# Optimization experiments

Measured on AMD Instinct MI355X. Metric: run time of the kernel, lower is better.

The kernel has to match this reference:

```python
import jax, jax.numpy as jnp
import numpy as np

BATCH = 524288
NUM_DRAFT = 128


def setup_inputs() -> dict:
    key = jax.random.key(0)
    k1, k2 = jax.random.split(key)
    seq_lens = jax.random.randint(k1, (BATCH,), 0, 8192, dtype=jnp.int32)
    evict_mask = jax.random.randint(k2, (BATCH, NUM_DRAFT), 0, 2, dtype=jnp.int32).astype(jnp.bool_)
    return {"seq_lens": seq_lens, "evict_mask": evict_mask, "page_size": 16}


def reference(seq_lens, evict_mask, page_size):
    # seq_lens: [B] int32, evict_mask: [B, D] bool, page_size: python int
    num_draft = evict_mask.shape[1]
    t = jnp.arange(num_draft, dtype=jnp.int32)          # [D]
    num_trues = jnp.sum(evict_mask.astype(jnp.int32), axis=1)   # [B]
    num_false = num_draft - num_trues                    # [B]
    # round (seq_len + num_false) up to page boundary, offset by seq_len
    start = (seq_lens + num_false - 1) // page_size * page_size - seq_lens  # [B]
    start_clamped = jnp.maximum(start, 0)                # [B]
    end = jnp.minimum(start + page_size, num_draft)      # [B] (uses unclamped start)
    range_mask = (t[None, :] >= start_clamped[:, None]) & (t[None, :] < end[:, None])  # [B, D]
    # kernel stores False where range_mask is True
    return jnp.where(range_mask, False, evict_mask)
```

## Files before the change

### kernel.cpp

```cpp
#include <hip/hip_runtime.h>


typedef int vint4 __attribute__((ext_vector_type(4)));

__global__ __launch_bounds__(256) void evict_range_kernel(
    const int* __restrict__ seq_lens,
    const int* __restrict__ evict_mask,
    const int* __restrict__ page_size_p,
    int* __restrict__ out,
    int batch)
{
    const int page = *page_size_p;
    const int lane32 = threadIdx.x & 31;
    const unsigned half_shift = threadIdx.x & 32;
    const int tid = blockIdx.x * blockDim.x + threadIdx.x;
    const int group = tid >> 5;
    const int ngroups = (gridDim.x * blockDim.x) >> 5;

    for (int row = group; row < batch; row += ngroups) {
        const vint4* mrow = reinterpret_cast<const vint4*>(evict_mask) + (size_t)row * 32;
        vint4 v = __builtin_nontemporal_load(&mrow[lane32]);

        unsigned long long b0 = __ballot(v.x != 0);
        unsigned long long b1 = __ballot(v.y != 0);
        unsigned long long b2 = __ballot(v.z != 0);
        unsigned long long b3 = __ballot(v.w != 0);
        int cnt = __popc((unsigned)(b0 >> half_shift))
                + __popc((unsigned)(b1 >> half_shift))
                + __popc((unsigned)(b2 >> half_shift))
                + __popc((unsigned)(b3 >> half_shift));

        int sl = seq_lens[row];
        int num_false = 128 - cnt;
        int s = sl + num_false - 1;
        int q = s / page;
        if (s < 0 && (s % page) != 0) q--;
        int start = q * page - sl;
        int sc  = start > 0 ? start : 0;
        int end = start + page;
        if (end > 128) end = 128;

        int t0 = lane32 * 4;
        vint4 o;
        o.x = (t0 + 0 >= sc && t0 + 0 < end) ? 0 : ((v.x != 0) ? 1 : 0);
        o.y = (t0 + 1 >= sc && t0 + 1 < end) ? 0 : ((v.y != 0) ? 1 : 0);
        o.z = (t0 + 2 >= sc && t0 + 2 < end) ? 0 : ((v.z != 0) ? 1 : 0);
        o.w = (t0 + 3 >= sc && t0 + 3 < end) ? 0 : ((v.w != 0) ? 1 : 0);
        __builtin_nontemporal_store(o, reinterpret_cast<vint4*>(out) + (size_t)row * 32 + lane32);
    }
}

extern "C" void kernel_launch(void* const* d_in, const int* in_sizes, int n_in,
                              void* d_out, int out_size, void* d_ws, size_t ws_size,
                              hipStream_t stream) {
    const int* seq_lens   = (const int*)d_in[0];
    const int* evict_mask = (const int*)d_in[1];
    const int* page_size  = (const int*)d_in[2];
    int* out = (int*)d_out;
    const int batch = in_sizes[0];

    const int blocks = 8192;
    evict_range_kernel<<<blocks, 256, 0, stream>>>(seq_lens, evict_mask, page_size, out, batch);
}
```

Measured before the change: 94.64 us.

## Process two rows per loop iteration, shift-divide for power-of-two pages, fewer blocks

The grid-stride loop now issues loads for two rows before processing either, which puts more memory requests in flight per wavefront. When the page size is a power of two, division is replaced by an arithmetic shift, which also floors correctly for negative values. The grid shrinks from 8192 to 2048 blocks, so each group of 32 threads handles more rows. Fewer resident waves could reduce latency hiding, but the doubled loads in flight are meant to make up for it.

```diff
diff --git a/kernel.cpp b/kernel.cpp
--- a/kernel.cpp
+++ b/kernel.cpp
@@ -2,6 +2,41 @@
 
 
 typedef int vint4 __attribute__((ext_vector_type(4)));
+
+__device__ __forceinline__ void process_row(
+    vint4 v, int sl, int page, int lgp, int lane32, unsigned half_shift,
+    int* __restrict__ out, size_t row)
+{
+    unsigned long long b0 = __ballot(v.x != 0);
+    unsigned long long b1 = __ballot(v.y != 0);
+    unsigned long long b2 = __ballot(v.z != 0);
+    unsigned long long b3 = __ballot(v.w != 0);
+    int cnt = __popc((unsigned)(b0 >> half_shift))
+            + __popc((unsigned)(b1 >> half_shift))
+            + __popc((unsigned)(b2 >> half_shift))
+            + __popc((unsigned)(b3 >> half_shift));
+
+    int s = sl + (128 - cnt) - 1;
+    int q;
+    if (lgp >= 0) {
+        q = s >> lgp;
+    } else {
+        q = s / page;
+        if (s < 0 && (s % page) != 0) q--;
+    }
+    int start = q * page - sl;
+    int sc  = start > 0 ? start : 0;
+    int end = start + page;
+    if (end > 128) end = 128;
+
+    int t0 = lane32 * 4;
+    vint4 o;
+    o.x = (t0 + 0 >= sc && t0 + 0 < end) ? 0 : ((v.x != 0) ? 1 : 0);
+    o.y = (t0 + 1 >= sc && t0 + 1 < end) ? 0 : ((v.y != 0) ? 1 : 0);
+    o.z = (t0 + 2 >= sc && t0 + 2 < end) ? 0 : ((v.z != 0) ? 1 : 0);
+    o.w = (t0 + 3 >= sc && t0 + 3 < end) ? 0 : ((v.w != 0) ? 1 : 0);
+    __builtin_nontemporal_store(o, reinterpret_cast<vint4*>(out) + row * 32 + lane32);
+}
 
 __global__ __launch_bounds__(256) void evict_range_kernel(
     const int* __restrict__ seq_lens,
@@ -11,42 +46,29 @@
     int batch)
 {
     const int page = *page_size_p;
+    const int lgp = ((page & (page - 1)) == 0) ? (31 - __clz(page)) : -1;
     const int lane32 = threadIdx.x & 31;
     const unsigned half_shift = threadIdx.x & 32;
     const int tid = blockIdx.x * blockDim.x + threadIdx.x;
     const int group = tid >> 5;
-    const int ngroups = (gridDim.x * blockDim.x) >> 5;
+    const int stride = (gridDim.x * blockDim.x) >> 5;
 
-    for (int row = group; row < batch; row += ngroups) {
-        const vint4* mrow = reinterpret_cast<const vint4*>(evict_mask) + (size_t)row * 32;
-        vint4 v = __builtin_nontemporal_load(&mrow[lane32]);
+    const vint4* mbase = reinterpret_cast<const vint4*>(evict_mask);
 
-        unsigned long long b0 = __ballot(v.x != 0);
-        unsigned long long b1 = __ballot(v.y != 0);
-        unsigned long long b2 = __ballot(v.z != 0);
-        unsigned long long b3 = __ballot(v.w != 0);
-        int cnt = __popc((unsigned)(b0 >> half_shift))
-                + __popc((unsigned)(b1 >> half_shift))
-                + __popc((unsigned)(b2 >> half_shift))
-                + __popc((unsigned)(b3 >> half_shift));
-
-        int sl = seq_lens[row];
-        int num_false = 128 - cnt;
-        int s = sl + num_false - 1;
-        int q = s / page;
-        if (s < 0 && (s % page) != 0) q--;
-        int start = q * page - sl;
-        int sc  = start > 0 ? start : 0;
-        int end = start + page;
-        if (end > 128) end = 128;
-
-        int t0 = lane32 * 4;
-        vint4 o;
-        o.x = (t0 + 0 >= sc && t0 + 0 < end) ? 0 : ((v.x != 0) ? 1 : 0);
-        o.y = (t0 + 1 >= sc && t0 + 1 < end) ? 0 : ((v.y != 0) ? 1 : 0);
-        o.z = (t0 + 2 >= sc && t0 + 2 < end) ? 0 : ((v.z != 0) ? 1 : 0);
-        o.w = (t0 + 3 >= sc && t0 + 3 < end) ? 0 : ((v.w != 0) ? 1 : 0);
-        __builtin_nontemporal_store(o, reinterpret_cast<vint4*>(out) + (size_t)row * 32 + lane32);
+    int row = group;
+    for (; row + stride < batch; row += 2 * stride) {
+        int rowB = row + stride;
+        vint4 vA = __builtin_nontemporal_load(mbase + (size_t)row  * 32 + lane32);
+        vint4 vB = __builtin_nontemporal_load(mbase + (size_t)rowB * 32 + lane32);
+        int slA = seq_lens[row];
+        int slB = seq_lens[rowB];
+        process_row(vA, slA, page, lgp, lane32, half_shift, out, (size_t)row);
+        process_row(vB, slB, page, lgp, lane32, half_shift, out, (size_t)rowB);
+    }
+    if (row < batch) {
+        vint4 vA = __builtin_nontemporal_load(mbase + (size_t)row * 32 + lane32);
+        int slA = seq_lens[row];
+        process_row(vA, slA, page, lgp, lane32, half_shift, out, (size_t)row);
     }
 }
 
@@ -59,6 +81,6 @@
     int* out = (int*)d_out;
     const int batch = in_sizes[0];
 
-    const int blocks = 8192;
+    const int blocks = 2048;
     evict_range_kernel<<<blocks, 256, 0, stream>>>(seq_lens, evict_mask, page_size, out, batch);
 }
```

Result: slower. 101.8 us (+7.6%).
